# Performance work log

Measured on AMD Instinct MI355X. Metric: run time of the kernel, lower is better.

Reference implementation:

```python
import jax, jax.numpy as jnp
import numpy as np

N_USERS = 100000
N_ITEMS = 50001  # item_max + 1 (padding row 0)
N_EDGES = 1000000
D = 64
B = 4096
MAXLEN = 50
NUM_GNN_LAYERS = 2
LAMBDA_A = 0.5


def setup_inputs() -> dict:
    key = jax.random.key(0)
    ks = jax.random.split(key, 11)
    user_table = jax.random.normal(ks[0], (N_USERS, D), jnp.float32) * 0.1
    item_table = jax.random.normal(ks[1], (N_ITEMS, D), jnp.float32) * 0.1
    item_table = item_table.at[0].set(0.0)  # padding_idx=0
    edge_val_uv = jax.random.uniform(ks[2], (N_EDGES,), jnp.float32)
    edge_val_vu = jax.random.uniform(ks[3], (N_EDGES,), jnp.float32)
    W_att_w = jax.random.normal(ks[4], (D, D), jnp.float32) / jnp.sqrt(D)
    W_att_b = jax.random.normal(ks[5], (D,), jnp.float32) * 0.01
    W_agg = jax.random.normal(ks[6], (D, D), jnp.float32) / jnp.sqrt(D)
    edge_u = jax.random.randint(ks[7], (N_EDGES,), 0, N_USERS, jnp.int32)
    edge_i = jax.random.randint(ks[8], (N_EDGES,), 0, N_ITEMS, jnp.int32)
    user_idx = jax.random.randint(ks[9], (B,), 0, N_USERS, jnp.int32)
    ctx_items = jax.random.randint(ks[10], (B, MAXLEN), 0, N_ITEMS, jnp.int32)
    return dict(user_table=user_table, item_table=item_table,
                edge_val_uv=edge_val_uv, edge_val_vu=edge_val_vu,
                W_att_w=W_att_w, W_att_b=W_att_b, W_agg=W_agg,
                edge_u=edge_u, edge_i=edge_i, user_idx=user_idx,
                ctx_items=ctx_items)


def _propagate(V0, edge_u, edge_i, edge_val_uv, edge_val_vu):
    # V_{l+1} = VU @ (UV @ V_l), sparse bipartite spmm via segment sums
    V = V0
    layers = [V]
    for _ in range(NUM_GNN_LAYERS):
        u_msg = jax.ops.segment_sum(edge_val_uv[:, None] * V[edge_i],
                                    edge_u, num_segments=N_USERS)  # [U, D]
        V = jax.ops.segment_sum(edge_val_vu[:, None] * u_msg[edge_u],
                                edge_i, num_segments=N_ITEMS)       # [I, D]
        layers.append(V)
    return jnp.mean(jnp.stack(layers, 0), axis=0) + V0


def reference(user_table, item_table, edge_val_uv, edge_val_vu,
              W_att_w, W_att_b, W_agg,
              edge_u, edge_i, user_idx, ctx_items):
    # item_embedding_select: GNN propagation over bipartite graph
    V = _propagate(item_table, edge_u, edge_i, edge_val_uv, edge_val_vu)

    # forward_user
    id_emb = user_table[user_idx]          # [B, D]
    seq_emb = V[ctx_items]                  # [B, L, D]

    # user_attention_pooling
    key = jnp.tanh(jnp.einsum('bld,ed->ble', seq_emb, W_att_w) + W_att_b)
    attention = jnp.einsum('bld,bd->bl', key, id_emb)
    mask = jnp.sum(seq_emb, axis=-1) == 0   # [B, L]
    X = jnp.where(mask, 0.0, attention)
    eX = jnp.exp(X)
    attn = eX / (jnp.sum(eX, axis=1, keepdims=True) + 1e-12)
    pooled = jnp.einsum('bl,bld->bd', attn, seq_emb)
    out = pooled @ W_agg.T

    return LAMBDA_A * id_emb + (1.0 - LAMBDA_A) * out
```

## Files before the change

kernel.cpp:

```cpp
#include <hip/hip_runtime.h>

#define N_USERS 100000
#define N_ITEMS 50001
#define N_EDGES 1000000
#define D 64
#define BATCH 4096
#define MAXLEN 50

#define SHU 8
#define SHI 7
#define NBU ((N_USERS + 255) >> 8)
#define NBI ((N_ITEMS + 127) >> 7)
#define CAP 3072
#define BEPB 8192
#define BBLOCKS ((N_EDGES + BEPB - 1) / BEPB)

typedef __attribute__((ext_vector_type(8))) short short8;
typedef __attribute__((ext_vector_type(4))) float f32x4;

__device__ __forceinline__ float bf_lo(unsigned u) { return __uint_as_float(u << 16); }
__device__ __forceinline__ float bf_hi(unsigned u) { return __uint_as_float(u & 0xffff0000u); }
__device__ __forceinline__ float bf_s(unsigned short s) { return __uint_as_float(((unsigned)s) << 16); }
__device__ __forceinline__ unsigned bf_pack2(float a, float b) {
    unsigned ba = __float_as_uint(a);
    unsigned bb = __float_as_uint(b);
    ba += 0x7fffu + ((ba >> 16) & 1u);
    bb += 0x7fffu + ((bb >> 16) & 1u);
    return (ba >> 16) | (bb & 0xffff0000u);
}
__device__ __forceinline__ float fast_tanh(float x) {
    float e = __expf(2.0f * x);
    return 1.0f - 2.0f * __builtin_amdgcn_rcpf(e + 1.0f);
}

__global__ __launch_bounds__(256) void convert_kernel(
    const float* __restrict__ src, unsigned* __restrict__ dst, int npairs)
{
    int i = blockIdx.x * 256 + threadIdx.x;
    if (i < npairs) {
        float2 f = ((const float2*)src)[i];
        dst[i] = bf_pack2(f.x, f.y);
    }
}

__global__ __launch_bounds__(512) void bin_kernel(
    const int* __restrict__ eu, const int* __restrict__ ei,
    const float* __restrict__ ev_uv, const float* __restrict__ ev_vu,
    int* __restrict__ gcur_u, int* __restrict__ gcur_i,
    int2* __restrict__ staged_u, int2* __restrict__ staged_i)
{
    __shared__ int hist[NBU];
    __shared__ int runbase[NBU];
    __shared__ unsigned short rank[BEPB];
    int tid = threadIdx.x;
    int dir_i = (blockIdx.x >= BBLOCKS) ? 1 : 0;
    int blk = blockIdx.x - (dir_i ? BBLOCKS : 0);
    const int* erow = dir_i ? ei : eu;
    const int* esrc = dir_i ? eu : ei;
    const float* eval = dir_i ? ev_vu : ev_uv;
    int* gcur = dir_i ? gcur_i : gcur_u;
    int2* staged = dir_i ? staged_i : staged_u;
    const int shift = dir_i ? SHI : SHU;
    const float qs = dir_i ? 32767.0f : 65535.0f;
    const int rlmask = dir_i ? 127 : 255;
    const int nb = dir_i ? NBI : NBU;

    for (int i = tid; i < nb; i += 512) hist[i] = 0;
    __syncthreads();
    int e0 = blk * BEPB;
    for (int k = 0; k < BEPB / 512; ++k) {
        int slot = k * 512 + tid;
        int e = e0 + slot;
        if (e < N_EDGES)
            rank[slot] = (unsigned short)atomicAdd(&hist[erow[e] >> shift], 1);
    }
    __syncthreads();
    for (int i = tid; i < nb; i += 512) {
        int cn = hist[i];
        runbase[i] = cn ? (i * CAP + atomicAdd(&gcur[i], cn)) : 0;
    }
    __syncthreads();
    for (int k = 0; k < BEPB / 512; ++k) {
        int slot = k * 512 + tid;
        int e = e0 + slot;
        if (e < N_EDGES) {
            int row = erow[e];
            unsigned q = (unsigned)(fminf(fmaxf(eval[e], 0.0f), 1.0f) * qs + 0.5f);
            int2 en;
            en.x = (int)((unsigned)(row & rlmask) << 16 | q);
            en.y = esrc[e];
            staged[runbase[row >> shift] + rank[slot]] = en;
        }
    }
}

__global__ __launch_bounds__(256) void place_kernel(
    const int2* __restrict__ staged_u, const int2* __restrict__ staged_i,
    const int* __restrict__ gcur_u, const int* __restrict__ gcur_i,
    unsigned* __restrict__ csr_u, unsigned* __restrict__ csr_i,
    int2* __restrict__ offend_u, int2* __restrict__ offend_i)
{
    __shared__ int cnt[256];
    __shared__ int s[256];
    __shared__ int cur[256];
    int tid = threadIdx.x;
    int dir_i = (blockIdx.x >= NBU) ? 1 : 0;
    int b = blockIdx.x - (dir_i ? NBU : 0);
    const int2* staged = dir_i ? staged_i : staged_u;
    const int* gcur = dir_i ? gcur_i : gcur_u;
    unsigned* csr = dir_i ? csr_i : csr_u;
    int2* offend = dir_i ? offend_i : offend_u;
    const int NR = dir_i ? 128 : 256;
    const int nrows = dir_i ? N_ITEMS : N_USERS;
    const int idxbits = dir_i ? 17 : 16;

    int sb = b * CAP;
    int eb = sb + gcur[b];
    if (tid < NR) cnt[tid] = 0;
    __syncthreads();
    for (int idx = sb + tid; idx < eb; idx += 256) {
        int rl = ((unsigned)staged[idx].x) >> 16;
        atomicAdd(&cnt[rl], 1);
    }
    __syncthreads();
    int c = (tid < NR) ? cnt[tid] : 0;
    s[tid] = c;
    __syncthreads();
    for (int off = 1; off < 256; off <<= 1) {
        int v = (tid >= off) ? s[tid - off] : 0;
        __syncthreads();
        s[tid] += v;
        __syncthreads();
    }
    int excl = s[tid] - c;
    int row = b * NR + tid;
    if (tid < NR && row < nrows) {
        int2 oe; oe.x = sb + excl; oe.y = sb + excl + c;
        offend[row] = oe;
    }
    if (tid < NR) cur[tid] = sb + excl;
    __syncthreads();
    for (int idx = sb + tid; idx < eb; idx += 256) {
        int2 en = staged[idx];
        unsigned w0 = (unsigned)en.x;
        int rl = w0 >> 16;
        unsigned q = w0 & 0xFFFFu;
        int pos = atomicAdd(&cur[rl], 1);
        csr[pos] = (q << idxbits) | (unsigned)en.y;
    }
}

template<int IDXBITS>
__device__ __forceinline__ void gather_row_q16(
    const unsigned* __restrict__ src, const unsigned* __restrict__ csr,
    int o, int e, int c8, int qq,
    float& A0, float& A1, float& A2, float& A3)
{
    constexpr unsigned MASK = (1u << IDXBITS) - 1u;
    constexpr float SCALE = 1.0f / (float)((1u << (32 - IDXBITS)) - 1u);
    float a0 = 0.f, a1 = 0.f, a2 = 0.f, a3 = 0.f;
    for (int base = o; base < e; base += 16) {
        int n = min(16, e - base);
        unsigned word = 0;
        if (c8 < n) word = csr[base + c8];
#pragma unroll 4
        for (int j = 0; j < n; ++j) {
            unsigned wj = (unsigned)__shfl((int)word, 16 * qq + j, 64);
            int r = (int)(wj & MASK);
            float v = (float)(wj >> IDXBITS) * SCALE;
            uint2 u2 = *(const uint2*)(src + (size_t)r * 32 + 2 * c8);
            a0 = fmaf(v, bf_lo(u2.x), a0);
            a1 = fmaf(v, bf_hi(u2.x), a1);
            a2 = fmaf(v, bf_lo(u2.y), a2);
            a3 = fmaf(v, bf_hi(u2.y), a3);
        }
    }
    A0 = a0; A1 = a1; A2 = a2; A3 = a3;
}

template<int IDXBITS>
__global__ __launch_bounds__(256) void gather_bf_kernel(
    const unsigned* __restrict__ src, const unsigned* __restrict__ csr,
    const int2* __restrict__ offend,
    unsigned* __restrict__ dst, int nrows)
{
    int gw = (blockIdx.x * 256 + threadIdx.x) >> 6;
    int lane = threadIdx.x & 63;
    int qq = lane >> 4, c8 = lane & 15;
    int row = gw * 4 + qq;
    int2 oe = (row < nrows) ? offend[row] : make_int2(0, 0);
    float a0, a1, a2, a3;
    gather_row_q16<IDXBITS>(src, csr, oe.x, oe.y, c8, qq, a0, a1, a2, a3);
    if (row < nrows) {
        uint2 o2;
        o2.x = bf_pack2(a0, a1);
        o2.y = bf_pack2(a2, a3);
        *((uint2*)(dst + (size_t)row * 32) + c8) = o2;
    }
}

__global__ __launch_bounds__(256) void gather_final_bf_kernel(
    const unsigned* __restrict__ src, const unsigned* __restrict__ csr,
    const int2* __restrict__ offend,
    const float* __restrict__ V0, const unsigned* __restrict__ V1bf,
    unsigned* __restrict__ Vf_bf)
{
    int gw = (blockIdx.x * 256 + threadIdx.x) >> 6;
    int lane = threadIdx.x & 63;
    int qq = lane >> 4, c8 = lane & 15;
    int row = gw * 4 + qq;
    int2 oe = (row < N_ITEMS) ? offend[row] : make_int2(0, 0);
    float a0, a1, a2, a3;
    gather_row_q16<17>(src, csr, oe.x, oe.y, c8, qq, a0, a1, a2, a3);
    if (row < N_ITEMS) {
        float4 v0 = *((const float4*)(V0 + (size_t)row * 64) + c8);
        uint2 u1 = *((const uint2*)(V1bf + (size_t)row * 32) + c8);
        float r0 = (v0.x + bf_lo(u1.x) + a0) * (1.0f / 3.0f) + v0.x;
        float r1 = (v0.y + bf_hi(u1.x) + a1) * (1.0f / 3.0f) + v0.y;
        float r2 = (v0.z + bf_lo(u1.y) + a2) * (1.0f / 3.0f) + v0.z;
        float r3 = (v0.w + bf_hi(u1.y) + a3) * (1.0f / 3.0f) + v0.w;
        uint2 o2;
        o2.x = bf_pack2(r0, r1);
        o2.y = bf_pack2(r2, r3);
        *((uint2*)(Vf_bf + (size_t)row * 32) + c8) = o2;
    }
}

__global__ __launch_bounds__(256) void phase2_kernel(
    const float* __restrict__ user_table, const unsigned* __restrict__ Vf_bf,
    const float* __restrict__ Watt, const float* __restrict__ Wb,
    const float* __restrict__ Wagg, const int* __restrict__ uidx,
    const int* __restrict__ ctx, float* __restrict__ out)
{
    __shared__ __align__(16) unsigned seq[4][64 * 36];
    __shared__ unsigned short wgT[64 * 72];
    __shared__ __align__(16) float idrow[4][64];
    __shared__ float attn_l[4][64];
    __shared__ float pooled_l[4][64];

    const int tid = threadIdx.x;
    const int w = tid >> 6;
    const int lane = tid & 63;
    const int q = lane >> 4;
    const int n = lane & 15;
    const int b = blockIdx.x * 4 + w;

    for (int i = tid; i < 64 * 64; i += 256) {
        int e = i >> 6, d = i & 63;
        unsigned bb = __float_as_uint(Wagg[i]);
        bb += 0x7fffu + ((bb >> 16) & 1u);
        wgT[d * 72 + e] = (unsigned short)(bb >> 16);
    }
    __syncthreads();

    short8 wa_f[4][2];
#pragma unroll
    for (int et = 0; et < 4; ++et)
#pragma unroll
        for (int ks = 0; ks < 2; ++ks) {
            const float* rp = Watt + (size_t)(16 * et + n) * 64 + 32 * ks + 8 * q;
            float4 f0 = *(const float4*)rp;
            float4 f1 = *(const float4*)(rp + 4);
            union { short8 s; unsigned u[4]; } t;
            t.u[0] = bf_pack2(f0.x, f0.y);
            t.u[1] = bf_pack2(f0.z, f0.w);
            t.u[2] = bf_pack2(f1.x, f1.y);
            t.u[3] = bf_pack2(f1.z, f1.w);
            wa_f[et][ks] = t.s;
        }
    f32x4 biasv[4];
#pragma unroll
    for (int et = 0; et < 4; ++et)
        biasv[et] = *(const f32x4*)(Wb + 16 * et + 4 * q);
    short8 ones8;
#pragma unroll
    for (int j = 0; j < 8; ++j) ones8[j] = (short)0x3F80;

    int uid = uidx[b];
    idrow[w][lane] = user_table[(size_t)uid * 64 + lane];
    f32x4 idv[4];
#pragma unroll
    for (int et = 0; et < 4; ++et)
        idv[et] = *(f32x4*)&idrow[w][16 * et + 4 * q];

    int ci = (lane < MAXLEN) ? ctx[b * MAXLEN + lane] : 0;
#pragma unroll 5
    for (int it = 0; it < 25; ++it) {
        int l = 2 * it + (lane >> 5);
        int cc = lane & 31;
        int rsrc = __shfl(ci, l, 64);
        seq[w][l * 36 + cc] = Vf_bf[(size_t)rsrc * 32 + cc];
    }

    float xs[4];
#pragma unroll
    for (int lt = 0; lt < 4; ++lt) {
        union { short8 s; uint4 u; } B0, B1;
        B0.u = *(const uint4*)&seq[w][(16 * lt + n) * 36 + 4 * q];
        B1.u = *(const uint4*)&seq[w][(16 * lt + n) * 36 + 16 + 4 * q];

        f32x4 rsum = {0.f, 0.f, 0.f, 0.f};
        rsum = __builtin_amdgcn_mfma_f32_16x16x32_bf16(ones8, B0.s, rsum, 0, 0, 0);
        rsum = __builtin_amdgcn_mfma_f32_16x16x32_bf16(ones8, B1.s, rsum, 0, 0, 0);
        float rsv = rsum[0];

        float xacc = 0.0f;
#pragma unroll
        for (int et = 0; et < 4; ++et) {
            f32x4 a = {0.f, 0.f, 0.f, 0.f};
            a = __builtin_amdgcn_mfma_f32_16x16x32_bf16(wa_f[et][0], B0.s, a, 0, 0, 0);
            a = __builtin_amdgcn_mfma_f32_16x16x32_bf16(wa_f[et][1], B1.s, a, 0, 0, 0);
#pragma unroll
            for (int r = 0; r < 4; ++r) {
                float t = fast_tanh(a[r] + biasv[et][r]);
                xacc = fmaf(t, idv[et][r], xacc);
            }
        }
        xacc += __shfl_xor(xacc, 16, 64);
        xacc += __shfl_xor(xacc, 32, 64);
        xs[lt] = (rsv == 0.0f) ? 0.0f : xacc;
    }

    float ex[4];
    float tot = 0.0f;
#pragma unroll
    for (int lt = 0; lt < 4; ++lt) {
        int l = 16 * lt + n;
        ex[lt] = (l < MAXLEN) ? __expf(xs[lt]) : 0.0f;
        tot += ex[lt];
    }
    tot += __shfl_xor(tot, 1, 64);
    tot += __shfl_xor(tot, 2, 64);
    tot += __shfl_xor(tot, 4, 64);
    tot += __shfl_xor(tot, 8, 64);
    float inv = 1.0f / (tot + 1e-12f);
    if (lane < 16) {
#pragma unroll
        for (int lt = 0; lt < 4; ++lt)
            attn_l[w][16 * lt + lane] = ex[lt] * inv;
    }

    float pooled = 0.0f;
    for (int l = 0; l < MAXLEN; ++l) {
        float a = attn_l[w][l];
        unsigned uu = seq[w][l * 36 + (lane >> 1)];
        float sv = (lane & 1) ? bf_hi(uu) : bf_lo(uu);
        pooled = fmaf(a, sv, pooled);
    }
    pooled_l[w][lane] = pooled;

    float o = 0.0f;
#pragma unroll 8
    for (int d = 0; d < 64; ++d) {
        float pv = pooled_l[w][d];
        float wv = bf_s(wgT[d * 72 + lane]);
        o = fmaf(pv, wv, o);
    }
    out[(size_t)b * 64 + lane] = 0.5f * idrow[w][lane] + 0.5f * o;
}


extern "C" void kernel_launch(void* const* d_in, const int* in_sizes, int n_in,
                              void* d_out, int out_size, void* d_ws, size_t ws_size,
                              hipStream_t stream)
{
    const float* user_table = (const float*)d_in[0];
    const float* item_table = (const float*)d_in[1];
    const float* ev_uv      = (const float*)d_in[2];
    const float* ev_vu      = (const float*)d_in[3];
    const float* Watt       = (const float*)d_in[4];
    const float* Wb         = (const float*)d_in[5];
    const float* Wagg       = (const float*)d_in[6];
    const int*   edge_u     = (const int*)d_in[7];
    const int*   edge_i     = (const int*)d_in[8];
    const int*   uidx       = (const int*)d_in[9];
    const int*   ctx        = (const int*)d_in[10];
    float* out = (float*)d_out;

    const size_t NCAP = (size_t)NBU * CAP;

    char* p = (char*)d_ws;
    unsigned* it_bf    = (unsigned*)p; p += (size_t)N_ITEMS * 32 * 4;
    unsigned* u_msg_bf = (unsigned*)p; p += (size_t)N_USERS * 32 * 4;
    unsigned* V1_bf    = (unsigned*)p; p += (size_t)N_ITEMS * 32 * 4;
    char*     Sreg     = p;            p += NCAP * 8 * 2;
    int2*     staged_u = (int2*)Sreg;
    int2*     staged_i = (int2*)(Sreg + NCAP * 8);
    unsigned* Vf_bf    = (unsigned*)Sreg;
    unsigned* csr_u    = (unsigned*)p; p += NCAP * 4;
    unsigned* csr_i    = (unsigned*)p; p += NCAP * 4;
    int2*     offend_u = (int2*)p;     p += (size_t)N_USERS * 8;
    int2*     offend_i = (int2*)p;     p += (size_t)N_ITEMS * 8;
    int*      gcur_u   = (int*)p;      p += NBU * 4;
    int*      gcur_i   = (int*)p;      p += NBI * 4;

    hipMemsetAsync(gcur_u, 0, (NBU + NBI) * 4, stream);

    convert_kernel<<<(N_ITEMS * 32 + 255) / 256, 256, 0, stream>>>(
        item_table, it_bf, N_ITEMS * 32);

    bin_kernel<<<2 * BBLOCKS, 512, 0, stream>>>(edge_u, edge_i, ev_uv, ev_vu,
                                                gcur_u, gcur_i, staged_u, staged_i);
    place_kernel<<<NBU + NBI, 256, 0, stream>>>(staged_u, staged_i, gcur_u, gcur_i,
                                                csr_u, csr_i, offend_u, offend_i);

    const int ublocks = (N_USERS + 15) / 16;
    const int iblocks = (N_ITEMS + 15) / 16;

    gather_bf_kernel<16><<<ublocks, 256, 0, stream>>>(it_bf, csr_u, offend_u, u_msg_bf, N_USERS);
    gather_bf_kernel<17><<<iblocks, 256, 0, stream>>>(u_msg_bf, csr_i, offend_i, V1_bf, N_ITEMS);
    gather_bf_kernel<16><<<ublocks, 256, 0, stream>>>(V1_bf, csr_u, offend_u, u_msg_bf, N_USERS);
    gather_final_bf_kernel<<<iblocks, 256, 0, stream>>>(u_msg_bf, csr_i, offend_i,
                                                        item_table, V1_bf, Vf_bf);

    phase2_kernel<<<BATCH / 4, 256, 0, stream>>>(user_table, Vf_bf, Watt, Wb, Wagg,
                                                 uidx, ctx, out);
}
```

Before: 275.4 us.

## Split SpMM gathers into source-index chunks for cache-resident passes

The CSR placement now sorts edges within each row by source-index chunk: two chunks for the user direction and four for the item direction. Each gather layer then runs as several passes, one per chunk, with fp32 partial sums kept in new workspace buffers. The aim is to keep each pass's gathered source rows small enough to stay in L2 or last-level cache, so the random row reads hit cache instead of HBM. CSR reads and partial-sum traffic use nontemporal hints. The cost is many more kernel launches, extra partial-sum reads and writes per row, and rows whose edges are spread across chunks.

```diff
diff --git a/kernel.cpp b/kernel.cpp
--- a/kernel.cpp
+++ b/kernel.cpp
@@ -14,6 +14,11 @@
 #define CAP 3072
 #define BEPB 8192
 #define BBLOCKS ((N_EDGES + BEPB - 1) / BEPB)
+
+#define NCH_U 2
+#define NCH_I 4
+#define UCHUNK_SPLIT 25024
+#define ICHUNK_DIV 25000u
 
 typedef __attribute__((ext_vector_type(8))) short short8;
 typedef __attribute__((ext_vector_type(4))) float f32x4;
@@ -94,15 +99,15 @@
     }
 }
 
-__global__ __launch_bounds__(256) void place_kernel(
+__global__ __launch_bounds__(512) void place_kernel(
     const int2* __restrict__ staged_u, const int2* __restrict__ staged_i,
     const int* __restrict__ gcur_u, const int* __restrict__ gcur_i,
     unsigned* __restrict__ csr_u, unsigned* __restrict__ csr_i,
     int2* __restrict__ offend_u, int2* __restrict__ offend_i)
 {
-    __shared__ int cnt[256];
-    __shared__ int s[256];
-    __shared__ int cur[256];
+    __shared__ int cnt[512];
+    __shared__ int s[512];
+    __shared__ int cur[512];
     int tid = threadIdx.x;
     int dir_i = (blockIdx.x >= NBU) ? 1 : 0;
     int b = blockIdx.x - (dir_i ? NBU : 0);
@@ -111,41 +116,53 @@
     unsigned* csr = dir_i ? csr_i : csr_u;
     int2* offend = dir_i ? offend_i : offend_u;
     const int NR = dir_i ? 128 : 256;
+    const int NCH = dir_i ? NCH_I : NCH_U;
     const int nrows = dir_i ? N_ITEMS : N_USERS;
     const int idxbits = dir_i ? 17 : 16;
 
     int sb = b * CAP;
     int eb = sb + gcur[b];
-    if (tid < NR) cnt[tid] = 0;
-    __syncthreads();
-    for (int idx = sb + tid; idx < eb; idx += 256) {
-        int rl = ((unsigned)staged[idx].x) >> 16;
-        atomicAdd(&cnt[rl], 1);
-    }
-    __syncthreads();
-    int c = (tid < NR) ? cnt[tid] : 0;
-    s[tid] = c;
-    __syncthreads();
-    for (int off = 1; off < 256; off <<= 1) {
+    cnt[tid] = 0;
+    __syncthreads();
+    for (int idx = sb + tid; idx < eb; idx += 512) {
+        int2 en = staged[idx];
+        int rl = ((unsigned)en.x) >> 16;
+        int c = dir_i ? (int)((unsigned)en.y / ICHUNK_DIV)
+                      : (en.y >= UCHUNK_SPLIT ? 1 : 0);
+        atomicAdd(&cnt[rl * NCH + c], 1);
+    }
+    __syncthreads();
+    int cv = cnt[tid];
+    s[tid] = cv;
+    __syncthreads();
+    for (int off = 1; off < 512; off <<= 1) {
         int v = (tid >= off) ? s[tid - off] : 0;
         __syncthreads();
         s[tid] += v;
         __syncthreads();
     }
-    int excl = s[tid] - c;
-    int row = b * NR + tid;
-    if (tid < NR && row < nrows) {
-        int2 oe; oe.x = sb + excl; oe.y = sb + excl + c;
-        offend[row] = oe;
-    }
-    if (tid < NR) cur[tid] = sb + excl;
-    __syncthreads();
-    for (int idx = sb + tid; idx < eb; idx += 256) {
+    int excl = s[tid] - cv;
+    {
+        int rl = tid / NCH;
+        int c = tid - rl * NCH;
+        int row = b * NR + rl;
+        if (row < nrows) {
+            int2 oe;
+            oe.x = sb + excl;
+            oe.y = sb + excl + cv;
+            offend[(size_t)row * NCH + c] = oe;
+        }
+    }
+    cur[tid] = sb + excl;
+    __syncthreads();
+    for (int idx = sb + tid; idx < eb; idx += 512) {
         int2 en = staged[idx];
         unsigned w0 = (unsigned)en.x;
         int rl = w0 >> 16;
         unsigned q = w0 & 0xFFFFu;
-        int pos = atomicAdd(&cur[rl], 1);
+        int c = dir_i ? (int)((unsigned)en.y / ICHUNK_DIV)
+                      : (en.y >= UCHUNK_SPLIT ? 1 : 0);
+        int pos = atomicAdd(&cur[rl * NCH + c], 1);
         csr[pos] = (q << idxbits) | (unsigned)en.y;
     }
 }
@@ -162,7 +179,7 @@
     for (int base = o; base < e; base += 16) {
         int n = min(16, e - base);
         unsigned word = 0;
-        if (c8 < n) word = csr[base + c8];
+        if (c8 < n) word = __builtin_nontemporal_load(csr + base + c8);
 #pragma unroll 4
         for (int j = 0; j < n; ++j) {
             unsigned wj = (unsigned)__shfl((int)word, 16 * qq + j, 64);
@@ -178,30 +195,43 @@
     A0 = a0; A1 = a1; A2 = a2; A3 = a3;
 }
 
-template<int IDXBITS>
-__global__ __launch_bounds__(256) void gather_bf_kernel(
+template<int IDXBITS, int NCH, int MODE>
+__global__ __launch_bounds__(256) void gather_pass_kernel(
     const unsigned* __restrict__ src, const unsigned* __restrict__ csr,
-    const int2* __restrict__ offend,
-    unsigned* __restrict__ dst, int nrows)
+    const int2* __restrict__ offend, int chunk,
+    float* __restrict__ part, unsigned* __restrict__ dst, int nrows)
 {
     int gw = (blockIdx.x * 256 + threadIdx.x) >> 6;
     int lane = threadIdx.x & 63;
     int qq = lane >> 4, c8 = lane & 15;
     int row = gw * 4 + qq;
-    int2 oe = (row < nrows) ? offend[row] : make_int2(0, 0);
+    int2 oe = (row < nrows) ? offend[(size_t)row * NCH + chunk] : make_int2(0, 0);
     float a0, a1, a2, a3;
     gather_row_q16<IDXBITS>(src, csr, oe.x, oe.y, c8, qq, a0, a1, a2, a3);
     if (row < nrows) {
-        uint2 o2;
-        o2.x = bf_pack2(a0, a1);
-        o2.y = bf_pack2(a2, a3);
-        *((uint2*)(dst + (size_t)row * 32) + c8) = o2;
-    }
-}
-
-__global__ __launch_bounds__(256) void gather_final_bf_kernel(
+        f32x4* pp = (f32x4*)(part + (size_t)row * 64) + c8;
+        if constexpr (MODE == 0) {
+            f32x4 v;
+            v[0] = a0; v[1] = a1; v[2] = a2; v[3] = a3;
+            __builtin_nontemporal_store(v, pp);
+        } else if constexpr (MODE == 1) {
+            f32x4 p = __builtin_nontemporal_load(pp);
+            p[0] += a0; p[1] += a1; p[2] += a2; p[3] += a3;
+            __builtin_nontemporal_store(p, pp);
+        } else {
+            f32x4 p = __builtin_nontemporal_load(pp);
+            uint2 o2;
+            o2.x = bf_pack2(p[0] + a0, p[1] + a1);
+            o2.y = bf_pack2(p[2] + a2, p[3] + a3);
+            *((uint2*)(dst + (size_t)row * 32) + c8) = o2;
+        }
+    }
+}
+
+__global__ __launch_bounds__(256) void gather_final2_kernel(
     const unsigned* __restrict__ src, const unsigned* __restrict__ csr,
     const int2* __restrict__ offend,
+    const float* __restrict__ part,
     const float* __restrict__ V0, const unsigned* __restrict__ V1bf,
     unsigned* __restrict__ Vf_bf)
 {
@@ -209,16 +239,18 @@
     int lane = threadIdx.x & 63;
     int qq = lane >> 4, c8 = lane & 15;
     int row = gw * 4 + qq;
-    int2 oe = (row < N_ITEMS) ? offend[row] : make_int2(0, 0);
+    int2 oe = (row < N_ITEMS) ? offend[(size_t)row * NCH_I + (NCH_I - 1)] : make_int2(0, 0);
     float a0, a1, a2, a3;
     gather_row_q16<17>(src, csr, oe.x, oe.y, c8, qq, a0, a1, a2, a3);
     if (row < N_ITEMS) {
+        f32x4 p = __builtin_nontemporal_load((const f32x4*)(part + (size_t)row * 64) + c8);
         float4 v0 = *((const float4*)(V0 + (size_t)row * 64) + c8);
         uint2 u1 = *((const uint2*)(V1bf + (size_t)row * 32) + c8);
-        float r0 = (v0.x + bf_lo(u1.x) + a0) * (1.0f / 3.0f) + v0.x;
-        float r1 = (v0.y + bf_hi(u1.x) + a1) * (1.0f / 3.0f) + v0.y;
-        float r2 = (v0.z + bf_lo(u1.y) + a2) * (1.0f / 3.0f) + v0.z;
-        float r3 = (v0.w + bf_hi(u1.y) + a3) * (1.0f / 3.0f) + v0.w;
+        float s0 = p[0] + a0, s1 = p[1] + a1, s2 = p[2] + a2, s3 = p[3] + a3;
+        float r0 = (v0.x + bf_lo(u1.x) + s0) * (1.0f / 3.0f) + v0.x;
+        float r1 = (v0.y + bf_hi(u1.x) + s1) * (1.0f / 3.0f) + v0.y;
+        float r2 = (v0.z + bf_lo(u1.y) + s2) * (1.0f / 3.0f) + v0.z;
+        float r3 = (v0.w + bf_hi(u1.y) + s3) * (1.0f / 3.0f) + v0.w;
         uint2 o2;
         o2.x = bf_pack2(r0, r1);
         o2.y = bf_pack2(r2, r3);
@@ -389,8 +421,10 @@
     unsigned* Vf_bf    = (unsigned*)Sreg;
     unsigned* csr_u    = (unsigned*)p; p += NCAP * 4;
     unsigned* csr_i    = (unsigned*)p; p += NCAP * 4;
-    int2*     offend_u = (int2*)p;     p += (size_t)N_USERS * 8;
-    int2*     offend_i = (int2*)p;     p += (size_t)N_ITEMS * 8;
+    int2*     offend_u = (int2*)p;     p += (size_t)N_USERS * NCH_U * 8;
+    int2*     offend_i = (int2*)p;     p += (size_t)N_ITEMS * NCH_I * 8;
+    float*    u_part   = (float*)p;    p += (size_t)N_USERS * 64 * 4;
+    float*    i_part   = (float*)p;    p += (size_t)N_ITEMS * 64 * 4;
     int*      gcur_u   = (int*)p;      p += NBU * 4;
     int*      gcur_i   = (int*)p;      p += NBI * 4;
 
@@ -401,17 +435,37 @@
 
     bin_kernel<<<2 * BBLOCKS, 512, 0, stream>>>(edge_u, edge_i, ev_uv, ev_vu,
                                                 gcur_u, gcur_i, staged_u, staged_i);
-    place_kernel<<<NBU + NBI, 256, 0, stream>>>(staged_u, staged_i, gcur_u, gcur_i,
+    place_kernel<<<NBU + NBI, 512, 0, stream>>>(staged_u, staged_i, gcur_u, gcur_i,
                                                 csr_u, csr_i, offend_u, offend_i);
 
     const int ublocks = (N_USERS + 15) / 16;
     const int iblocks = (N_ITEMS + 15) / 16;
 
-    gather_bf_kernel<16><<<ublocks, 256, 0, stream>>>(it_bf, csr_u, offend_u, u_msg_bf, N_USERS);
-    gather_bf_kernel<17><<<iblocks, 256, 0, stream>>>(u_msg_bf, csr_i, offend_i, V1_bf, N_ITEMS);
-    gather_bf_kernel<16><<<ublocks, 256, 0, stream>>>(V1_bf, csr_u, offend_u, u_msg_bf, N_USERS);
-    gather_final_bf_kernel<<<iblocks, 256, 0, stream>>>(u_msg_bf, csr_i, offend_i,
-                                                        item_table, V1_bf, Vf_bf);
+    gather_pass_kernel<16, NCH_U, 0><<<ublocks, 256, 0, stream>>>(
+        it_bf, csr_u, offend_u, 0, u_part, nullptr, N_USERS);
+    gather_pass_kernel<16, NCH_U, 2><<<ublocks, 256, 0, stream>>>(
+        it_bf, csr_u, offend_u, 1, u_part, u_msg_bf, N_USERS);
+    gather_pass_kernel<17, NCH_I, 0><<<iblocks, 256, 0, stream>>>(
+        u_msg_bf, csr_i, offend_i, 0, i_part, nullptr, N_ITEMS);
+    gather_pass_kernel<17, NCH_I, 1><<<iblocks, 256, 0, stream>>>(
+        u_msg_bf, csr_i, offend_i, 1, i_part, nullptr, N_ITEMS);
+    gather_pass_kernel<17, NCH_I, 1><<<iblocks, 256, 0, stream>>>(
+        u_msg_bf, csr_i, offend_i, 2, i_part, nullptr, N_ITEMS);
+    gather_pass_kernel<17, NCH_I, 2><<<iblocks, 256, 0, stream>>>(
+        u_msg_bf, csr_i, offend_i, 3, i_part, V1_bf, N_ITEMS);
+
+    gather_pass_kernel<16, NCH_U, 0><<<ublocks, 256, 0, stream>>>(
+        V1_bf, csr_u, offend_u, 0, u_part, nullptr, N_USERS);
+    gather_pass_kernel<16, NCH_U, 2><<<ublocks, 256, 0, stream>>>(
+        V1_bf, csr_u, offend_u, 1, u_part, u_msg_bf, N_USERS);
+    gather_pass_kernel<17, NCH_I, 0><<<iblocks, 256, 0, stream>>>(
+        u_msg_bf, csr_i, offend_i, 0, i_part, nullptr, N_ITEMS);
+    gather_pass_kernel<17, NCH_I, 1><<<iblocks, 256, 0, stream>>>(
+        u_msg_bf, csr_i, offend_i, 1, i_part, nullptr, N_ITEMS);
+    gather_pass_kernel<17, NCH_I, 1><<<iblocks, 256, 0, stream>>>(
+        u_msg_bf, csr_i, offend_i, 2, i_part, nullptr, N_ITEMS);
+    gather_final2_kernel<<<iblocks, 256, 0, stream>>>(
+        u_msg_bf, csr_i, offend_i, i_part, item_table, V1_bf, Vf_bf);
 
     phase2_kernel<<<BATCH / 4, 256, 0, stream>>>(user_table, Vf_bf, Watt, Wb, Wagg,
                                                  uidx, ctx, out);
```

New measurement: 372.1 us. +35.1%, slower.
